# Kernel tuning notes

Measured on AMD Instinct MI355X. Metric: run time of the kernel, lower is better.

The kernel has to match this reference:

```python
import jax, jax.numpy as jnp
import numpy as np

NUM_CLASSES = 5
TRANSITION_PENALTY = 0.1
SMOOTHING = 0.1


def _make_transition_matrix(c: int) -> jnp.ndarray:
    i = np.arange(c)[:, None]
    j = np.arange(c)[None, :]
    d = np.abs(i - j)
    t = np.where(d == 0, 0.0, np.where(d == 1, 0.5, np.where(d == 2, 1.0, 2.0)))
    return jnp.asarray(t, dtype=jnp.float32)


def setup_inputs() -> dict:
    key = jax.random.key(0)
    k1, k2 = jax.random.split(key)
    B = 4194304
    inputs = jax.random.normal(k1, (B, NUM_CLASSES), dtype=jnp.float32)
    targets = jax.random.randint(k2, (B,), 0, NUM_CLASSES, dtype=jnp.int32)
    return {"inputs": inputs, "targets": targets}


def reference(inputs, targets):
    c = NUM_CLASSES
    log_probs = jax.nn.log_softmax(inputs, axis=-1)  # [B, C]
    # label-smoothing CE: smooth target dist has (1-s) on target, s/(C-1) elsewhere
    onehot = jax.nn.one_hot(targets, c, dtype=log_probs.dtype)
    smooth = SMOOTHING / (c - 1)
    smooth_targets = onehot * (1.0 - SMOOTHING - smooth) + smooth
    ce_loss = (-(smooth_targets * log_probs).sum(axis=-1)).mean()
    # transition penalty: mean_i sum_j softmax(inputs)[i,j] * T[targets[i], j]
    probs = jnp.exp(log_probs)
    T = _make_transition_matrix(c)
    penalty = (probs * T[targets]).sum(axis=-1).mean()
    return ce_loss + TRANSITION_PENALTY * penalty
```

## Files before the change

kernel.cpp:

```cpp
#include <hip/hip_runtime.h>


constexpr int C = 5;

__device__ __forceinline__ float trans_w(int d) {
    d = d < 0 ? -d : d;
    return (d == 0) ? 0.0f : (d == 1) ? 0.5f : (d == 2) ? 1.0f : 2.0f;
}

__device__ __forceinline__ float row_loss(const float a[C], int t) {
    float m = fmaxf(fmaxf(fmaxf(a[0], a[1]), fmaxf(a[2], a[3])), a[4]);
    float e0 = __expf(a[0] - m);
    float e1 = __expf(a[1] - m);
    float e2 = __expf(a[2] - m);
    float e3 = __expf(a[3] - m);
    float e4 = __expf(a[4] - m);
    float s  = e0 + e1 + e2 + e3 + e4;
    float ls = __logf(s);
    float inv = 1.0f / s;

    float lp0 = a[0] - m - ls;
    float lp1 = a[1] - m - ls;
    float lp2 = a[2] - m - ls;
    float lp3 = a[3] - m - ls;
    float lp4 = a[4] - m - ls;
    float sumlp = lp0 + lp1 + lp2 + lp3 + lp4;

    float lpt = (t == 0) ? lp0 : (t == 1) ? lp1 : (t == 2) ? lp2 : (t == 3) ? lp3 : lp4;

    float pen = e0 * trans_w(t - 0) + e1 * trans_w(t - 1) + e2 * trans_w(t - 2)
              + e3 * trans_w(t - 3) + e4 * trans_w(t - 4);
    pen *= inv;

    float ce = -(0.875f * lpt + 0.025f * sumlp);
    return ce + 0.1f * pen;
}

__global__ __launch_bounds__(256) void bloom_reduce(const float* __restrict__ x,
                                                    const int* __restrict__ tgt,
                                                    double* __restrict__ acc,
                                                    int nGroups) {
    int g = blockIdx.x * blockDim.x + threadIdx.x;
    float local = 0.0f;
    if (g < nGroups) {
        const float4* x4 = (const float4*)x;
        float4 v0 = x4[g * 5 + 0];
        float4 v1 = x4[g * 5 + 1];
        float4 v2 = x4[g * 5 + 2];
        float4 v3 = x4[g * 5 + 3];
        float4 v4 = x4[g * 5 + 4];
        int4 t4 = ((const int4*)tgt)[g];

        float r0[C] = {v0.x, v0.y, v0.z, v0.w, v1.x};
        float r1[C] = {v1.y, v1.z, v1.w, v2.x, v2.y};
        float r2[C] = {v2.z, v2.w, v3.x, v3.y, v3.z};
        float r3[C] = {v3.w, v4.x, v4.y, v4.z, v4.w};

        local  = row_loss(r0, t4.x);
        local += row_loss(r1, t4.y);
        local += row_loss(r2, t4.z);
        local += row_loss(r3, t4.w);
    }

    #pragma unroll
    for (int off = 32; off > 0; off >>= 1)
        local += __shfl_down(local, off, 64);

    __shared__ float wsum[4];
    int lane = threadIdx.x & 63;
    int wid  = threadIdx.x >> 6;
    if (lane == 0) wsum[wid] = local;
    __syncthreads();
    if (threadIdx.x == 0) {
        double bs = (double)wsum[0] + (double)wsum[1] + (double)wsum[2] + (double)wsum[3];
        atomicAdd(acc, bs);
    }
}

__global__ void bloom_finalize(const double* __restrict__ acc,
                               const float* __restrict__ x,
                               const int* __restrict__ tgt,
                               float* __restrict__ out,
                               int tailStart, int B) {
    double s = acc[0];
    for (int r = tailStart; r < B; ++r) {
        float a[C];
        #pragma unroll
        for (int j = 0; j < C; ++j) a[j] = x[r * C + j];
        s += (double)row_loss(a, tgt[r]);
    }
    out[0] = (float)(s / (double)B);
}

extern "C" void kernel_launch(void* const* d_in, const int* in_sizes, int n_in,
                              void* d_out, int out_size, void* d_ws, size_t ws_size,
                              hipStream_t stream) {
    const float* x  = (const float*)d_in[0];
    const int* tgt  = (const int*)d_in[1];
    float* out      = (float*)d_out;
    double* acc     = (double*)d_ws;

    int B = in_sizes[1];
    int nGroups = B / 4;
    int tailStart = nGroups * 4;

    hipMemsetAsync(d_ws, 0, sizeof(double), stream);

    int threads = 256;
    int blocks = (nGroups + threads - 1) / threads;
    if (blocks < 1) blocks = 1;
    bloom_reduce<<<blocks, threads, 0, stream>>>(x, tgt, acc, nGroups);
    bloom_finalize<<<1, 1, 0, stream>>>(acc, x, tgt, out, tailStart, B);
}
```

Measured before the change: 163.2 us.

## Fuse reduce and finalize with last-block reduction, coalesced LDS-staged loads, persistent grid

```diff
diff --git a/kernel.cpp b/kernel.cpp
--- a/kernel.cpp
+++ b/kernel.cpp
@@ -2,113 +2,148 @@
 
 
 constexpr int C = 5;
+constexpr int BLOCK = 256;
+constexpr int ROWS_PER_TILE = 4 * BLOCK;
+constexpr int F4_PER_TILE = ROWS_PER_TILE * C / 4;
+constexpr int NBLOCKS = 1024;
 
 __device__ __forceinline__ float trans_w(int d) {
     d = d < 0 ? -d : d;
     return (d == 0) ? 0.0f : (d == 1) ? 0.5f : (d == 2) ? 1.0f : 2.0f;
 }
 
-__device__ __forceinline__ float row_loss(const float a[C], int t) {
-    float m = fmaxf(fmaxf(fmaxf(a[0], a[1]), fmaxf(a[2], a[3])), a[4]);
-    float e0 = __expf(a[0] - m);
-    float e1 = __expf(a[1] - m);
-    float e2 = __expf(a[2] - m);
-    float e3 = __expf(a[3] - m);
-    float e4 = __expf(a[4] - m);
+__device__ __forceinline__ float row_loss(float a0, float a1, float a2,
+                                          float a3, float a4, int t) {
+    float m = fmaxf(fmaxf(fmaxf(a0, a1), fmaxf(a2, a3)), a4);
+    float e0 = __expf(a0 - m);
+    float e1 = __expf(a1 - m);
+    float e2 = __expf(a2 - m);
+    float e3 = __expf(a3 - m);
+    float e4 = __expf(a4 - m);
     float s  = e0 + e1 + e2 + e3 + e4;
     float ls = __logf(s);
     float inv = 1.0f / s;
 
-    float lp0 = a[0] - m - ls;
-    float lp1 = a[1] - m - ls;
-    float lp2 = a[2] - m - ls;
-    float lp3 = a[3] - m - ls;
-    float lp4 = a[4] - m - ls;
+    float lp0 = a0 - m - ls;
+    float lp1 = a1 - m - ls;
+    float lp2 = a2 - m - ls;
+    float lp3 = a3 - m - ls;
+    float lp4 = a4 - m - ls;
     float sumlp = lp0 + lp1 + lp2 + lp3 + lp4;
+    float lpt = (t == 0) ? lp0 : (t == 1) ? lp1 : (t == 2) ? lp2
+              : (t == 3) ? lp3 : lp4;
 
-    float lpt = (t == 0) ? lp0 : (t == 1) ? lp1 : (t == 2) ? lp2 : (t == 3) ? lp3 : lp4;
-
-    float pen = e0 * trans_w(t - 0) + e1 * trans_w(t - 1) + e2 * trans_w(t - 2)
+    float pen = e0 * trans_w(t)     + e1 * trans_w(t - 1) + e2 * trans_w(t - 2)
               + e3 * trans_w(t - 3) + e4 * trans_w(t - 4);
     pen *= inv;
 
-    float ce = -(0.875f * lpt + 0.025f * sumlp);
-    return ce + 0.1f * pen;
+    return -(0.875f * lpt + 0.025f * sumlp) + 0.1f * pen;
 }
 
-__global__ __launch_bounds__(256) void bloom_reduce(const float* __restrict__ x,
-                                                    const int* __restrict__ tgt,
-                                                    double* __restrict__ acc,
-                                                    int nGroups) {
-    int g = blockIdx.x * blockDim.x + threadIdx.x;
+__global__ __launch_bounds__(BLOCK) void bloom_fused(
+        const float* __restrict__ x, const int* __restrict__ tgt,
+        double* __restrict__ partial, unsigned int* __restrict__ counter,
+        float* __restrict__ out, int nTiles, int B) {
+    __shared__ float4 tile4[F4_PER_TILE];
+    __shared__ double wsum[4];
+    __shared__ double dsum[4];
+    __shared__ bool isLast;
+
+    const int tid = threadIdx.x;
+    const float4* __restrict__ x4 = (const float4*)x;
+    const int4* __restrict__ tgt4 = (const int4*)tgt;
+
     float local = 0.0f;
-    if (g < nGroups) {
-        const float4* x4 = (const float4*)x;
-        float4 v0 = x4[g * 5 + 0];
-        float4 v1 = x4[g * 5 + 1];
-        float4 v2 = x4[g * 5 + 2];
-        float4 v3 = x4[g * 5 + 3];
-        float4 v4 = x4[g * 5 + 4];
-        int4 t4 = ((const int4*)tgt)[g];
 
-        float r0[C] = {v0.x, v0.y, v0.z, v0.w, v1.x};
-        float r1[C] = {v1.y, v1.z, v1.w, v2.x, v2.y};
-        float r2[C] = {v2.z, v2.w, v3.x, v3.y, v3.z};
-        float r3[C] = {v3.w, v4.x, v4.y, v4.z, v4.w};
+    for (int tile = blockIdx.x; tile < nTiles; tile += gridDim.x) {
+        const long base4 = (long)tile * F4_PER_TILE;
+        float4 v0 = x4[base4 + 0 * BLOCK + tid];
+        float4 v1 = x4[base4 + 1 * BLOCK + tid];
+        float4 v2 = x4[base4 + 2 * BLOCK + tid];
+        float4 v3 = x4[base4 + 3 * BLOCK + tid];
+        float4 v4 = x4[base4 + 4 * BLOCK + tid];
+        int4 t4 = tgt4[(long)tile * BLOCK + tid];
 
-        local  = row_loss(r0, t4.x);
-        local += row_loss(r1, t4.y);
-        local += row_loss(r2, t4.z);
-        local += row_loss(r3, t4.w);
+        tile4[0 * BLOCK + tid] = v0;
+        tile4[1 * BLOCK + tid] = v1;
+        tile4[2 * BLOCK + tid] = v2;
+        tile4[3 * BLOCK + tid] = v3;
+        tile4[4 * BLOCK + tid] = v4;
+        __syncthreads();
+
+        float4 r0 = tile4[tid * 5 + 0];
+        float4 r1 = tile4[tid * 5 + 1];
+        float4 r2 = tile4[tid * 5 + 2];
+        float4 r3 = tile4[tid * 5 + 3];
+        float4 r4 = tile4[tid * 5 + 4];
+
+        local += row_loss(r0.x, r0.y, r0.z, r0.w, r1.x, t4.x);
+        local += row_loss(r1.y, r1.z, r1.w, r2.x, r2.y, t4.y);
+        local += row_loss(r2.z, r2.w, r3.x, r3.y, r3.z, t4.z);
+        local += row_loss(r3.w, r4.x, r4.y, r4.z, r4.w, t4.w);
+        __syncthreads();
+    }
+
+    if (blockIdx.x == gridDim.x - 1) {
+        for (int r = nTiles * ROWS_PER_TILE + tid; r < B; r += BLOCK) {
+            local += row_loss(x[(long)r * C + 0], x[(long)r * C + 1],
+                              x[(long)r * C + 2], x[(long)r * C + 3],
+                              x[(long)r * C + 4], tgt[r]);
+        }
     }
 
     #pragma unroll
     for (int off = 32; off > 0; off >>= 1)
         local += __shfl_down(local, off, 64);
+    const int lane = tid & 63;
+    const int wid = tid >> 6;
+    if (lane == 0) wsum[wid] = (double)local;
+    __syncthreads();
 
-    __shared__ float wsum[4];
-    int lane = threadIdx.x & 63;
-    int wid  = threadIdx.x >> 6;
-    if (lane == 0) wsum[wid] = local;
+    if (tid == 0) {
+        double bs = wsum[0] + wsum[1] + wsum[2] + wsum[3];
+        atomicExch((unsigned long long*)&partial[blockIdx.x],
+                   (unsigned long long)__double_as_longlong(bs));
+        __threadfence();
+        unsigned prev = atomicAdd(counter, 1u);
+        isLast = (prev == (unsigned)(gridDim.x - 1));
+    }
     __syncthreads();
-    if (threadIdx.x == 0) {
-        double bs = (double)wsum[0] + (double)wsum[1] + (double)wsum[2] + (double)wsum[3];
-        atomicAdd(acc, bs);
+
+    if (isLast) {
+        double s = 0.0;
+        for (int i = tid; i < (int)gridDim.x; i += BLOCK) {
+            unsigned long long bits =
+                atomicAdd((unsigned long long*)&partial[i], 0ull);
+            s += __longlong_as_double((long long)bits);
+        }
+        #pragma unroll
+        for (int off = 32; off > 0; off >>= 1)
+            s += __shfl_down(s, off, 64);
+        if (lane == 0) dsum[wid] = s;
+        __syncthreads();
+        if (tid == 0)
+            out[0] = (float)((dsum[0] + dsum[1] + dsum[2] + dsum[3]) / (double)B);
     }
-}
-
-__global__ void bloom_finalize(const double* __restrict__ acc,
-                               const float* __restrict__ x,
-                               const int* __restrict__ tgt,
-                               float* __restrict__ out,
-                               int tailStart, int B) {
-    double s = acc[0];
-    for (int r = tailStart; r < B; ++r) {
-        float a[C];
-        #pragma unroll
-        for (int j = 0; j < C; ++j) a[j] = x[r * C + j];
-        s += (double)row_loss(a, tgt[r]);
-    }
-    out[0] = (float)(s / (double)B);
 }
 
 extern "C" void kernel_launch(void* const* d_in, const int* in_sizes, int n_in,
                               void* d_out, int out_size, void* d_ws, size_t ws_size,
                               hipStream_t stream) {
-    const float* x  = (const float*)d_in[0];
-    const int* tgt  = (const int*)d_in[1];
-    float* out      = (float*)d_out;
-    double* acc     = (double*)d_ws;
+    const float* x = (const float*)d_in[0];
+    const int* tgt = (const int*)d_in[1];
+    float* out = (float*)d_out;
 
     int B = in_sizes[1];
-    int nGroups = B / 4;
-    int tailStart = nGroups * 4;
+    int nTiles = B / ROWS_PER_TILE;
+    int blocks = NBLOCKS;
+    if (nTiles < blocks) blocks = (nTiles > 0) ? nTiles : 1;
 
-    hipMemsetAsync(d_ws, 0, sizeof(double), stream);
+    double* partial = (double*)d_ws;
+    unsigned int* counter = (unsigned int*)((char*)d_ws + blocks * sizeof(double));
 
-    int threads = 256;
-    int blocks = (nGroups + threads - 1) / threads;
-    if (blocks < 1) blocks = 1;
-    bloom_reduce<<<blocks, threads, 0, stream>>>(x, tgt, acc, nGroups);
-    bloom_finalize<<<1, 1, 0, stream>>>(acc, x, tgt, out, tailStart, B);
+    hipMemsetAsync(counter, 0, sizeof(unsigned int), stream);
+
+    bloom_fused<<<blocks, BLOCK, 0, stream>>>(x, tgt, partial, counter, out,
+                                              nTiles, B);
 }
```

After: 172.4 us. 5.6% more time.
